# Kernel optimization log

Hardware: AMD Instinct MI355X
Metric: run time of the kernel (lower is better)

Reference implementation:

```python
import jax, jax.numpy as jnp
import numpy as np

B, LQ, LP, H, D = 64, 32, 256, 768, 128
EPS = 1e-12


def setup_inputs() -> dict:
    key = jax.random.key(0)
    ks = jax.random.split(key, 7)
    query_hidden = jax.random.normal(ks[0], (B, LQ, H), dtype=jnp.float32)
    positive_hidden = jax.random.normal(ks[1], (B, LP, H), dtype=jnp.float32)
    negative_hidden = jax.random.normal(ks[2], (B, LP, H), dtype=jnp.float32)
    W = jax.random.normal(ks[3], (H, D), dtype=jnp.float32) * 0.02
    b = jax.random.normal(ks[4], (D,), dtype=jnp.float32) * 0.02
    pos_mask = jax.random.randint(ks[5], (B, LP), 0, 2).astype(bool)
    neg_mask = jax.random.randint(ks[6], (B, LP), 0, 2).astype(bool)
    # guarantee every passage has at least one filtered token (ragged lists are non-empty)
    pos_mask = pos_mask.at[:, 0].set(True)
    neg_mask = neg_mask.at[:, 0].set(True)
    return {
        'query_hidden': query_hidden,
        'positive_hidden': positive_hidden,
        'negative_hidden': negative_hidden,
        'W': W,
        'b': b,
        'positive_filter_mask': pos_mask,
        'negative_filter_mask': neg_mask,
    }


def _encode(h, W, b):
    # linear projection then F.normalize (torch default dim=1 -> TOKEN axis)
    x = h @ W + b  # [B, L, D]
    norm = jnp.linalg.norm(x, axis=1, keepdims=True)  # over token axis, faithful to dim=1
    return x / jnp.maximum(norm, EPS)


def _late_interaction(q, p, mask):
    # q: [B, LQ, D], p: [B, LP, D], mask: [B, LP] bool
    sims = jnp.einsum('bqd,cpd->bcqp', q, p)  # [B, B, LQ, LP]
    sims = jnp.where(mask[None, :, None, :], sims, -jnp.inf)
    return sims.max(axis=3).sum(axis=2)  # MaxSim: max over passage tokens, sum over query tokens -> [B, B]


def reference(query_hidden, positive_hidden, negative_hidden, W, b,
              positive_filter_mask, negative_filter_mask):
    qv = _encode(query_hidden, W, b)
    pv = _encode(positive_hidden, W, b)
    nv = _encode(negative_hidden, W, b)
    pos_scores = _late_interaction(qv, pv, positive_filter_mask)
    neg_scores = _late_interaction(qv, nv, negative_filter_mask)
    return jnp.concatenate([pos_scores, neg_scores], axis=1)  # [B, 2B]
```

## Files before the change

kernel.cpp:

```cpp
#include <hip/hip_runtime.h>

typedef __attribute__((ext_vector_type(4))) float f32x4;
typedef __attribute__((ext_vector_type(8))) short s16x8;
typedef __attribute__((ext_vector_type(4))) short s16x4;
typedef __attribute__((ext_vector_type(8))) __bf16 bf16x8;

#define B_ 64
#define LQ_ 32
#define LP_ 256
#define H_ 768
#define D_ 128

__device__ __forceinline__ short cvt_bf16(float f) {
  unsigned u = __builtin_bit_cast(unsigned, f);
  unsigned r = (u + 0x7fffu + ((u >> 16) & 1u)) >> 16;
  return (short)r;
}
__device__ __forceinline__ float frombf(short h) {
  unsigned v = ((unsigned)(unsigned short)h) << 16;
  return __builtin_bit_cast(float, v);
}
__device__ __forceinline__ f32x4 mfma16(s16x8 a, s16x8 b, f32x4 c) {
  return __builtin_amdgcn_mfma_f32_16x16x32_bf16(
      __builtin_bit_cast(bf16x8, a), __builtin_bit_cast(bf16x8, b), c, 0, 0, 0);
}

__global__ __launch_bounds__(256) void k_pre(const float* __restrict__ W,
                                             const int* __restrict__ pm,
                                             const int* __restrict__ nm,
                                             short* __restrict__ Wt,
                                             float* __restrict__ mf) {
  __shared__ float tile[32][33];
  int bid = blockIdx.x;
  int t = threadIdx.x;
  if (bid < 96) {
    int k0 = (bid % 24) * 32, n0 = (bid / 24) * 32;
    int r = t >> 3, c4 = (t & 7) << 2;
    f32x4 v = *(const f32x4*)(W + (size_t)(k0 + r) * D_ + n0 + c4);
    tile[r][c4 + 0] = v[0]; tile[r][c4 + 1] = v[1];
    tile[r][c4 + 2] = v[2]; tile[r][c4 + 3] = v[3];
    __syncthreads();
    s16x4 o;
    o[0] = cvt_bf16(tile[c4 + 0][r]);
    o[1] = cvt_bf16(tile[c4 + 1][r]);
    o[2] = cvt_bf16(tile[c4 + 2][r]);
    o[3] = cvt_bf16(tile[c4 + 3][r]);
    *(s16x4*)(Wt + (size_t)(n0 + r) * H_ + k0 + c4) = o;
  } else {
    int i = (bid - 96) * 256 + t;
    float ninf = -__builtin_inff();
    mf[i]         = pm[i] ? 0.f : ninf;
    mf[16384 + i] = nm[i] ? 0.f : ninf;
  }
}

__global__ __launch_bounds__(256, 4) void k_proj(
    const float* __restrict__ Hq, const float* __restrict__ Hp, const float* __restrict__ Hn,
    const short* __restrict__ Wt, const float* __restrict__ bias,
    short* __restrict__ Xq, short* __restrict__ Xp, short* __restrict__ Xn,
    float* __restrict__ ps) {
  __shared__ short As[32 * 64];
  __shared__ short Bs[128 * 64];
  __shared__ float psum[2][128];
  int bid = blockIdx.x;
  const float* Hs; short* X; int row0;
  if (bid < 64)       { Hs = Hq; X = Xq; row0 = bid * 32; }
  else if (bid < 576) { Hs = Hp; X = Xp; row0 = (bid - 64) * 32; }
  else                { Hs = Hn; X = Xn; row0 = (bid - 576) * 32; }
  int t = threadIdx.x, lane = t & 63, w = t >> 6;
  int wm = w >> 1, wn = w & 1, lhi = lane >> 4, llo = lane & 15;

  int ar = t >> 3, akc = (t & 7) << 3;
  int br = t >> 1, bkc = (t & 1) << 5;
  const float* aptr = Hs + (size_t)(row0 + ar) * H_ + akc;
  const short* bptr = Wt + (size_t)br * H_ + bkc;
  int ast = (ar * 128 + akc * 2) ^ ((ar & 7) << 4);
  int bst = (br * 128 + bkc * 2);
  int bswz = ((br & 7) << 4);
  char* Ab = (char*)As; char* Bb = (char*)Bs;

  int arow = wm * 16 + llo;
  int aoff0 = (arow * 128 + lhi * 16) ^ ((arow & 7) << 4);
  int aoff1 = (arow * 128 + 64 + lhi * 16) ^ ((arow & 7) << 4);
  int boff[4][2];
  for (int ni = 0; ni < 4; ni++) {
    int brow = wn * 64 + ni * 16 + llo;
    boff[ni][0] = (brow * 128 + lhi * 16) ^ ((brow & 7) << 4);
    boff[ni][1] = (brow * 128 + 64 + lhi * 16) ^ ((brow & 7) << 4);
  }

  f32x4 pa0 = *(const f32x4*)(aptr);
  f32x4 pa1 = *(const f32x4*)(aptr + 4);
  s16x8 pb0 = *(const s16x8*)(bptr);
  s16x8 pb1 = *(const s16x8*)(bptr + 8);
  s16x8 pb2 = *(const s16x8*)(bptr + 16);
  s16x8 pb3 = *(const s16x8*)(bptr + 24);

  f32x4 acc[4] = {};
  for (int it = 0; it < 12; ++it) {
    s16x8 av;
    av[0] = cvt_bf16(pa0[0]); av[1] = cvt_bf16(pa0[1]);
    av[2] = cvt_bf16(pa0[2]); av[3] = cvt_bf16(pa0[3]);
    av[4] = cvt_bf16(pa1[0]); av[5] = cvt_bf16(pa1[1]);
    av[6] = cvt_bf16(pa1[2]); av[7] = cvt_bf16(pa1[3]);
    *(s16x8*)(Ab + ast) = av;
    *(s16x8*)(Bb + ((bst +  0) ^ bswz)) = pb0;
    *(s16x8*)(Bb + ((bst + 16) ^ bswz)) = pb1;
    *(s16x8*)(Bb + ((bst + 32) ^ bswz)) = pb2;
    *(s16x8*)(Bb + ((bst + 48) ^ bswz)) = pb3;
    asm volatile("s_waitcnt lgkmcnt(0)" ::: "memory");
    __builtin_amdgcn_s_barrier();
    if (it < 11) {
      const float* ap = aptr + (it + 1) * 64;
      pa0 = *(const f32x4*)(ap);
      pa1 = *(const f32x4*)(ap + 4);
      const short* bp = bptr + (it + 1) * 64;
      pb0 = *(const s16x8*)(bp);
      pb1 = *(const s16x8*)(bp + 8);
      pb2 = *(const s16x8*)(bp + 16);
      pb3 = *(const s16x8*)(bp + 24);
    }
    s16x8 af0 = *(const s16x8*)(Ab + aoff0);
    s16x8 af1 = *(const s16x8*)(Ab + aoff1);
    s16x8 bf0[4], bf1[4];
    for (int ni = 0; ni < 4; ni++) bf0[ni] = *(const s16x8*)(Bb + boff[ni][0]);
    for (int ni = 0; ni < 4; ni++) bf1[ni] = *(const s16x8*)(Bb + boff[ni][1]);
    for (int ni = 0; ni < 4; ni++) acc[ni] = mfma16(af0, bf0[ni], acc[ni]);
    for (int ni = 0; ni < 4; ni++) acc[ni] = mfma16(af1, bf1[ni], acc[ni]);
    __builtin_amdgcn_sched_barrier(0);
    __builtin_amdgcn_s_barrier();
  }

  for (int ni = 0; ni < 4; ni++) {
    int col = wn * 64 + ni * 16 + llo;
    float bv = bias[col];
    float s = 0.f;
    for (int r = 0; r < 4; r++) {
      float xv = acc[ni][r] + bv;
      s += xv * xv;
      X[(size_t)(row0 + wm * 16 + lhi * 4 + r) * D_ + col] = cvt_bf16(xv);
    }
    s += __shfl_xor(s, 16, 64);
    s += __shfl_xor(s, 32, 64);
    if (lhi == 0) psum[wm][col] = s;
  }
  __syncthreads();
  if (t < 128) ps[(size_t)bid * 128 + t] = psum[0][t] + psum[1][t];
}

__global__ __launch_bounds__(256) void k_normfin(
    const short* __restrict__ Xq, const short* __restrict__ Xp, const short* __restrict__ Xn,
    const float* __restrict__ ps,
    short* __restrict__ Vq, short* __restrict__ Vp, short* __restrict__ Vn) {
  __shared__ float invs[128];
  int bid = blockIdx.x;
  const short* X; short* V; int row0, pbase, pcnt;
  if (bid < 64)       { X = Xq; V = Vq; row0 = bid * 32;         pbase = bid;                          pcnt = 1; }
  else if (bid < 576) { X = Xp; V = Vp; row0 = (bid - 64) * 32;  pbase = 64 + ((bid - 64) & ~7);       pcnt = 8; }
  else                { X = Xn; V = Vn; row0 = (bid - 576) * 32; pbase = 576 + ((bid - 576) & ~7);     pcnt = 8; }
  int t = threadIdx.x;
  if (t < 128) {
    float s = 0.f;
    for (int j = 0; j < pcnt; j++) s += ps[(size_t)(pbase + j) * 128 + t];
    invs[t] = 1.0f / fmaxf(sqrtf(s), 1e-12f);
  }
  __syncthreads();
  int row = row0 + (t >> 3), c0 = (t & 7) << 4;
  const short* xr = X + (size_t)row * D_ + c0;
  s16x8 x0 = *(const s16x8*)(xr);
  s16x8 x1 = *(const s16x8*)(xr + 8);
  f32x4 i0 = *(const f32x4*)(&invs[c0]);
  f32x4 i1 = *(const f32x4*)(&invs[c0 + 4]);
  f32x4 i2 = *(const f32x4*)(&invs[c0 + 8]);
  f32x4 i3 = *(const f32x4*)(&invs[c0 + 12]);
  s16x8 o0, o1;
  for (int j = 0; j < 4; j++) {
    o0[j]     = cvt_bf16(frombf(x0[j])     * i0[j]);
    o0[j + 4] = cvt_bf16(frombf(x0[j + 4]) * i1[j]);
    o1[j]     = cvt_bf16(frombf(x1[j])     * i2[j]);
    o1[j + 4] = cvt_bf16(frombf(x1[j + 4]) * i3[j]);
  }
  short* vr = V + (size_t)row * D_ + c0;
  *(s16x8*)(vr) = o0;
  *(s16x8*)(vr + 8) = o1;
}

__global__ __launch_bounds__(512, 2) void k_maxsim(
    const short* __restrict__ QV, const short* __restrict__ PV, const short* __restrict__ NV,
    const float* __restrict__ MF, float* __restrict__ OUT) {
  __shared__ short Ps[LP_ * D_];
  int t = threadIdx.x, lane = t & 63, w = t >> 6;
  int lhi = lane >> 4, llo = lane & 15;
  int c = blockIdx.x, side = blockIdx.y, quarter = blockIdx.z;
  const short* P = side ? NV : PV;
  const float* mfb = MF + (size_t)(side * B_ + c) * LP_;

  const short* qb = QV + (size_t)(quarter * 512 + w * 64) * D_;
  s16x8 bq[4][4];
  for (int ni = 0; ni < 4; ni++)
    for (int ks = 0; ks < 4; ks++)
      bq[ni][ks] = *(const s16x8*)(qb + (size_t)(ni * 16 + llo) * D_ + ks * 32 + lhi * 8);

  const short* src = P + (size_t)c * LP_ * D_;
  for (int i = 0; i < 8; i++) {
    int s = i * 512 + t;
    int p = s >> 4, kc = s & 15;
    s16x8 v = *(const s16x8*)(src + (size_t)p * D_ + kc * 8);
    int byteoff = (p * 256 + kc * 16) ^ ((p & 7) << 4);
    *(s16x8*)((char*)Ps + byteoff) = v;
  }
  __syncthreads();

  float ninf = -__builtin_inff();
  float rmax[4] = {ninf, ninf, ninf, ninf};
  for (int pi = 0; pi < 4; pi++) {
    f32x4 acc[4][4] = {};
    for (int ks = 0; ks < 4; ks++) {
      s16x8 pa[4];
      for (int mi = 0; mi < 4; mi++) {
        int prow = pi * 64 + mi * 16 + llo;
        int off = (prow * 256 + ks * 64 + lhi * 16) ^ ((prow & 7) << 4);
        pa[mi] = *(const s16x8*)((char*)Ps + off);
      }
      __builtin_amdgcn_s_setprio(1);
      for (int mi = 0; mi < 4; mi++)
        for (int ni = 0; ni < 4; ni++)
          acc[mi][ni] = mfma16(pa[mi], bq[ni][ks], acc[mi][ni]);
      __builtin_amdgcn_s_setprio(0);
    }
    f32x4 mk[4];
    for (int mi = 0; mi < 4; mi++)
      mk[mi] = *(const f32x4*)(mfb + pi * 64 + mi * 16 + lhi * 4);
    for (int ni = 0; ni < 4; ni++)
      for (int mi = 0; mi < 4; mi++)
        for (int r = 0; r < 4; r++)
          rmax[ni] = fmaxf(rmax[ni], acc[mi][ni][r] + mk[mi][r]);
  }
  for (int ni = 0; ni < 4; ni++) {
    rmax[ni] = fmaxf(rmax[ni], __shfl_xor(rmax[ni], 16, 64));
    rmax[ni] = fmaxf(rmax[ni], __shfl_xor(rmax[ni], 32, 64));
  }
  float s0 = rmax[0] + rmax[1];
  float s1 = rmax[2] + rmax[3];
  for (int m = 1; m < 16; m <<= 1) {
    s0 += __shfl_xor(s0, m, 64);
    s1 += __shfl_xor(s1, m, 64);
  }
  if (lane == 0) {
    int b0 = quarter * 16 + w * 2;
    OUT[(size_t)b0 * 128 + side * 64 + c] = s0;
    OUT[(size_t)(b0 + 1) * 128 + side * 64 + c] = s1;
  }
}

extern "C" void kernel_launch(void* const* d_in, const int* in_sizes, int n_in,
                              void* d_out, int out_size, void* d_ws, size_t ws_size,
                              hipStream_t stream) {
  const float* qh = (const float*)d_in[0];
  const float* ph = (const float*)d_in[1];
  const float* nh = (const float*)d_in[2];
  const float* W  = (const float*)d_in[3];
  const float* bias = (const float*)d_in[4];
  const int* pm = (const int*)d_in[5];
  const int* nm = (const int*)d_in[6];
  float* out = (float*)d_out;
  char* ws = (char*)d_ws;

  short* Wt = (short*)(ws + 0x0);
  float* mf = (float*)(ws + 0x30000);
  float* ps = (float*)(ws + 0x50000);
  short* xq = (short*)(ws + 0xE0000);
  short* xp = (short*)(ws + 0x160000);
  short* xn = (short*)(ws + 0x560000);
  short* qv = (short*)(ws + 0x960000);
  short* pv = (short*)(ws + 0x9E0000);
  short* nv = (short*)(ws + 0xDE0000);

  k_pre<<<160, 256, 0, stream>>>(W, pm, nm, Wt, mf);
  k_proj<<<1088, 256, 0, stream>>>(qh, ph, nh, Wt, bias, xq, xp, xn, ps);
  k_normfin<<<1088, 256, 0, stream>>>(xq, xp, xn, ps, qv, pv, nv);
  k_maxsim<<<dim3(64, 2, 4), 512, 0, stream>>>(qv, pv, nv, mf, out);
}
```

Measured before the change: 64.48 us.

## Rewrite projection as single-wave blocks loading operands directly into registers

The projection kernel drops shared-memory staging and barriers. Each block becomes one 64-thread wave computing a 16x128 tile, reading A (fp32 rows) and W^T fragments from global memory straight into MFMA operand registers, with a one-step register prefetch. Partial norm sums are now written per 16-row block, so the normalisation kernel's partial-sum indexing and the workspace offsets change to match. The goal is to remove LDS traffic and synchronisation overhead. In exchange, W is reloaded from global or L2 by every block with no sharing between waves, and each block loses per-block reuse.

```diff
diff --git a/kernel.cpp b/kernel.cpp
--- a/kernel.cpp
+++ b/kernel.cpp
@@ -23,6 +23,18 @@
 __device__ __forceinline__ f32x4 mfma16(s16x8 a, s16x8 b, f32x4 c) {
   return __builtin_amdgcn_mfma_f32_16x16x32_bf16(
       __builtin_bit_cast(bf16x8, a), __builtin_bit_cast(bf16x8, b), c, 0, 0, 0);
+}
+__device__ __forceinline__ s16x8 cvt8(f32x4 a, f32x4 b) {
+  s16x8 r;
+  r[0] = __builtin_bit_cast(short, (__bf16)a[0]);
+  r[1] = __builtin_bit_cast(short, (__bf16)a[1]);
+  r[2] = __builtin_bit_cast(short, (__bf16)a[2]);
+  r[3] = __builtin_bit_cast(short, (__bf16)a[3]);
+  r[4] = __builtin_bit_cast(short, (__bf16)b[0]);
+  r[5] = __builtin_bit_cast(short, (__bf16)b[1]);
+  r[6] = __builtin_bit_cast(short, (__bf16)b[2]);
+  r[7] = __builtin_bit_cast(short, (__bf16)b[3]);
+  return r;
 }
 
 __global__ __launch_bounds__(256) void k_pre(const float* __restrict__ W,
@@ -54,98 +66,57 @@
   }
 }
 
-__global__ __launch_bounds__(256, 4) void k_proj(
+__global__ __launch_bounds__(64) void k_proj(
     const float* __restrict__ Hq, const float* __restrict__ Hp, const float* __restrict__ Hn,
     const short* __restrict__ Wt, const float* __restrict__ bias,
     short* __restrict__ Xq, short* __restrict__ Xp, short* __restrict__ Xn,
     float* __restrict__ ps) {
-  __shared__ short As[32 * 64];
-  __shared__ short Bs[128 * 64];
-  __shared__ float psum[2][128];
-  int bid = blockIdx.x;
+  int g = blockIdx.x;
   const float* Hs; short* X; int row0;
-  if (bid < 64)       { Hs = Hq; X = Xq; row0 = bid * 32; }
-  else if (bid < 576) { Hs = Hp; X = Xp; row0 = (bid - 64) * 32; }
-  else                { Hs = Hn; X = Xn; row0 = (bid - 576) * 32; }
-  int t = threadIdx.x, lane = t & 63, w = t >> 6;
-  int wm = w >> 1, wn = w & 1, lhi = lane >> 4, llo = lane & 15;
-
-  int ar = t >> 3, akc = (t & 7) << 3;
-  int br = t >> 1, bkc = (t & 1) << 5;
-  const float* aptr = Hs + (size_t)(row0 + ar) * H_ + akc;
-  const short* bptr = Wt + (size_t)br * H_ + bkc;
-  int ast = (ar * 128 + akc * 2) ^ ((ar & 7) << 4);
-  int bst = (br * 128 + bkc * 2);
-  int bswz = ((br & 7) << 4);
-  char* Ab = (char*)As; char* Bb = (char*)Bs;
-
-  int arow = wm * 16 + llo;
-  int aoff0 = (arow * 128 + lhi * 16) ^ ((arow & 7) << 4);
-  int aoff1 = (arow * 128 + 64 + lhi * 16) ^ ((arow & 7) << 4);
-  int boff[4][2];
-  for (int ni = 0; ni < 4; ni++) {
-    int brow = wn * 64 + ni * 16 + llo;
-    boff[ni][0] = (brow * 128 + lhi * 16) ^ ((brow & 7) << 4);
-    boff[ni][1] = (brow * 128 + 64 + lhi * 16) ^ ((brow & 7) << 4);
-  }
-
+  if (g < 128)       { Hs = Hq; X = Xq; row0 = g * 16; }
+  else if (g < 1152) { Hs = Hp; X = Xp; row0 = (g - 128) * 16; }
+  else               { Hs = Hn; X = Xn; row0 = (g - 1152) * 16; }
+  int lane = threadIdx.x;
+  int lhi = lane >> 4, llo = lane & 15;
+
+  const float* aptr = Hs + (size_t)(row0 + llo) * H_ + lhi * 8;
+  const short* bptr = Wt + (size_t)llo * H_ + lhi * 8;
+
+  f32x4 acc[8] = {};
   f32x4 pa0 = *(const f32x4*)(aptr);
   f32x4 pa1 = *(const f32x4*)(aptr + 4);
-  s16x8 pb0 = *(const s16x8*)(bptr);
-  s16x8 pb1 = *(const s16x8*)(bptr + 8);
-  s16x8 pb2 = *(const s16x8*)(bptr + 16);
-  s16x8 pb3 = *(const s16x8*)(bptr + 24);
-
-  f32x4 acc[4] = {};
-  for (int it = 0; it < 12; ++it) {
-    s16x8 av;
-    av[0] = cvt_bf16(pa0[0]); av[1] = cvt_bf16(pa0[1]);
-    av[2] = cvt_bf16(pa0[2]); av[3] = cvt_bf16(pa0[3]);
-    av[4] = cvt_bf16(pa1[0]); av[5] = cvt_bf16(pa1[1]);
-    av[6] = cvt_bf16(pa1[2]); av[7] = cvt_bf16(pa1[3]);
-    *(s16x8*)(Ab + ast) = av;
-    *(s16x8*)(Bb + ((bst +  0) ^ bswz)) = pb0;
-    *(s16x8*)(Bb + ((bst + 16) ^ bswz)) = pb1;
-    *(s16x8*)(Bb + ((bst + 32) ^ bswz)) = pb2;
-    *(s16x8*)(Bb + ((bst + 48) ^ bswz)) = pb3;
-    asm volatile("s_waitcnt lgkmcnt(0)" ::: "memory");
-    __builtin_amdgcn_s_barrier();
-    if (it < 11) {
-      const float* ap = aptr + (it + 1) * 64;
+  s16x8 pb[8];
+  for (int ni = 0; ni < 8; ni++)
+    pb[ni] = *(const s16x8*)(bptr + (size_t)ni * 16 * H_);
+
+  for (int it = 0; it < 24; ++it) {
+    s16x8 af = cvt8(pa0, pa1);
+    s16x8 bq[8];
+    for (int ni = 0; ni < 8; ni++) bq[ni] = pb[ni];
+    if (it < 23) {
+      const float* ap = aptr + (it + 1) * 32;
       pa0 = *(const f32x4*)(ap);
       pa1 = *(const f32x4*)(ap + 4);
-      const short* bp = bptr + (it + 1) * 64;
-      pb0 = *(const s16x8*)(bp);
-      pb1 = *(const s16x8*)(bp + 8);
-      pb2 = *(const s16x8*)(bp + 16);
-      pb3 = *(const s16x8*)(bp + 24);
+      const short* bp = bptr + (it + 1) * 32;
+      for (int ni = 0; ni < 8; ni++)
+        pb[ni] = *(const s16x8*)(bp + (size_t)ni * 16 * H_);
     }
-    s16x8 af0 = *(const s16x8*)(Ab + aoff0);
-    s16x8 af1 = *(const s16x8*)(Ab + aoff1);
-    s16x8 bf0[4], bf1[4];
-    for (int ni = 0; ni < 4; ni++) bf0[ni] = *(const s16x8*)(Bb + boff[ni][0]);
-    for (int ni = 0; ni < 4; ni++) bf1[ni] = *(const s16x8*)(Bb + boff[ni][1]);
-    for (int ni = 0; ni < 4; ni++) acc[ni] = mfma16(af0, bf0[ni], acc[ni]);
-    for (int ni = 0; ni < 4; ni++) acc[ni] = mfma16(af1, bf1[ni], acc[ni]);
-    __builtin_amdgcn_sched_barrier(0);
-    __builtin_amdgcn_s_barrier();
-  }
-
-  for (int ni = 0; ni < 4; ni++) {
-    int col = wn * 64 + ni * 16 + llo;
+    for (int ni = 0; ni < 8; ni++) acc[ni] = mfma16(af, bq[ni], acc[ni]);
+  }
+
+  for (int ni = 0; ni < 8; ni++) {
+    int col = ni * 16 + llo;
     float bv = bias[col];
     float s = 0.f;
     for (int r = 0; r < 4; r++) {
       float xv = acc[ni][r] + bv;
       s += xv * xv;
-      X[(size_t)(row0 + wm * 16 + lhi * 4 + r) * D_ + col] = cvt_bf16(xv);
+      X[(size_t)(row0 + lhi * 4 + r) * D_ + col] = cvt_bf16(xv);
     }
     s += __shfl_xor(s, 16, 64);
     s += __shfl_xor(s, 32, 64);
-    if (lhi == 0) psum[wm][col] = s;
-  }
-  __syncthreads();
-  if (t < 128) ps[(size_t)bid * 128 + t] = psum[0][t] + psum[1][t];
+    if (lhi == 0) ps[(size_t)g * 128 + col] = s;
+  }
 }
 
 __global__ __launch_bounds__(256) void k_normfin(
@@ -155,9 +126,9 @@
   __shared__ float invs[128];
   int bid = blockIdx.x;
   const short* X; short* V; int row0, pbase, pcnt;
-  if (bid < 64)       { X = Xq; V = Vq; row0 = bid * 32;         pbase = bid;                          pcnt = 1; }
-  else if (bid < 576) { X = Xp; V = Vp; row0 = (bid - 64) * 32;  pbase = 64 + ((bid - 64) & ~7);       pcnt = 8; }
-  else                { X = Xn; V = Vn; row0 = (bid - 576) * 32; pbase = 576 + ((bid - 576) & ~7);     pcnt = 8; }
+  if (bid < 64)       { X = Xq; V = Vq; row0 = bid * 32;         pbase = bid * 2;                         pcnt = 2;  }
+  else if (bid < 576) { X = Xp; V = Vp; row0 = (bid - 64) * 32;  pbase = 128 + ((bid - 64) / 8) * 16;     pcnt = 16; }
+  else                { X = Xn; V = Vn; row0 = (bid - 576) * 32; pbase = 1152 + ((bid - 576) / 8) * 16;   pcnt = 16; }
   int t = threadIdx.x;
   if (t < 128) {
     float s = 0.f;
@@ -269,15 +240,15 @@
   short* Wt = (short*)(ws + 0x0);
   float* mf = (float*)(ws + 0x30000);
   float* ps = (float*)(ws + 0x50000);
-  short* xq = (short*)(ws + 0xE0000);
-  short* xp = (short*)(ws + 0x160000);
-  short* xn = (short*)(ws + 0x560000);
-  short* qv = (short*)(ws + 0x960000);
-  short* pv = (short*)(ws + 0x9E0000);
-  short* nv = (short*)(ws + 0xDE0000);
+  short* xq = (short*)(ws + 0x160000);
+  short* xp = (short*)(ws + 0x1E0000);
+  short* xn = (short*)(ws + 0x5E0000);
+  short* qv = (short*)(ws + 0x9E0000);
+  short* pv = (short*)(ws + 0xA60000);
+  short* nv = (short*)(ws + 0xE60000);
 
   k_pre<<<160, 256, 0, stream>>>(W, pm, nm, Wt, mf);
-  k_proj<<<1088, 256, 0, stream>>>(qh, ph, nh, Wt, bias, xq, xp, xn, ps);
+  k_proj<<<2176, 64, 0, stream>>>(qh, ph, nh, Wt, bias, xq, xp, xn, ps);
   k_normfin<<<1088, 256, 0, stream>>>(xq, xp, xn, ps, qv, pv, nv);
   k_maxsim<<<dim3(64, 2, 4), 512, 0, stream>>>(qv, pv, nv, mf, out);
 }
```

Measured after the change: 103.7 us. 60.8% more time.
